# Optimization experiments

Measured on AMD Instinct MI355X. Metric: run time of the kernel, lower is better.

## Reference

```python
import jax, jax.numpy as jnp
import numpy as np

CODEBOOK_SIZE = 32768
EMBED_DIM = 4


def setup_inputs() -> dict:
    key = jax.random.key(0)
    k1, k2 = jax.random.split(key)
    # [batch, temporal, channels, height, width]
    hidden_state = jax.random.normal(k1, (1, 4, EMBED_DIM, 48, 48), dtype=jnp.float32)
    # nn.Embedding weight, init uniform(-1/cb, 1/cb) as in the torch module
    embedding = jax.random.uniform(
        k2, (CODEBOOK_SIZE, EMBED_DIM), dtype=jnp.float32,
        minval=-1.0 / CODEBOOK_SIZE, maxval=1.0 / CODEBOOK_SIZE,
    )
    return {"hidden_state": hidden_state, "embedding": embedding}


def reference(hidden_state, embedding):
    b, t, c, h, w = hidden_state.shape
    # permute channels last, flatten to [N, C]
    x = jnp.transpose(hidden_state, (0, 1, 3, 4, 2)).reshape(-1, c)
    distances = (
        jnp.sum(x * x, axis=1, keepdims=True)
        + jnp.sum(embedding * embedding, axis=1)
        - 2.0 * jnp.einsum("nd,kd->nk", x, embedding)
    )
    min_encoding_indices = jnp.argmin(distances, axis=1)
    return min_encoding_indices.reshape(b, t, h, w)
```

## Files before the change

### kernel.cpp

```cpp
#include <hip/hip_runtime.h>
#include <cfloat>


#define ROWS   9
#define BLOCK  256
#define NK     32768
#define EPT    2
#define CHUNK  (BLOCK * EPT)

__global__ __launch_bounds__(BLOCK, 2)
void vq_argmin_kernel(const float* __restrict__ hs,
                      const float4* __restrict__ cb,
                      int* __restrict__ out)
{
    __shared__ float sRD[4 * ROWS];
    __shared__ int   sRI[4 * ROWS];

    const int tid = threadIdx.x;
    const int rowbase = blockIdx.x * ROWS;

    float xr0[ROWS], xr1[ROWS], xr2[ROWS], xr3[ROWS];
    float x2[ROWS];
    float best[ROWS];
    int   bidx[ROWS];

    #pragma unroll
    for (int r = 0; r < ROWS; ++r) {
        int n = rowbase + r;
        int t = n / 2304;
        int rem = n - t * 2304;
        const float* p = hs + t * 9216 + rem;
        float a0 = p[0], a1 = p[2304], a2 = p[4608], a3 = p[6912];
        xr0[r] = a0; xr1[r] = a1; xr2[r] = a2; xr3[r] = a3;
        x2[r] = __fadd_rn(__fadd_rn(__fadd_rn(__fmul_rn(a0, a0),
                                              __fmul_rn(a1, a1)),
                                    __fmul_rn(a2, a2)),
                          __fmul_rn(a3, a3));
        best[r] = FLT_MAX;
        bidx[r] = 0;
    }

    float4 bufA[EPT], bufB[EPT];

    auto load_chunk = [&](float4* buf, int tb) {
        #pragma unroll
        for (int j = 0; j < EPT; ++j) buf[j] = cb[tb + tid + j * BLOCK];
    };
    auto compute_chunk = [&](const float4* buf, int tb) {
        #pragma unroll
        for (int j = 0; j < EPT; ++j) {
            float4 e = buf[j];
            float e2v = __fadd_rn(__fadd_rn(__fadd_rn(__fmul_rn(e.x, e.x),
                                                      __fmul_rn(e.y, e.y)),
                                            __fmul_rn(e.z, e.z)),
                                  __fmul_rn(e.w, e.w));
            int kk = tb + tid + j * BLOCK;
            #pragma unroll
            for (int r = 0; r < ROWS; ++r) {
                float dot = __builtin_fmaf(xr3[r], e.w,
                            __builtin_fmaf(xr2[r], e.z,
                            __builtin_fmaf(xr1[r], e.y,
                            __fmul_rn(xr0[r], e.x))));
                float t1 = __fadd_rn(x2[r], e2v);
                float d  = __builtin_fmaf(dot, -2.0f, t1);
                if (d < best[r]) { best[r] = d; bidx[r] = kk; }
            }
        }
    };

    load_chunk(bufA, 0);
    for (int tb = 0; tb < NK; tb += 2 * CHUNK) {
        load_chunk(bufB, tb + CHUNK);
        compute_chunk(bufA, tb);
        int nb = tb + 2 * CHUNK < NK ? tb + 2 * CHUNK : 0;
        load_chunk(bufA, nb);
        compute_chunk(bufB, tb + CHUNK);
    }

    #pragma unroll
    for (int r = 0; r < ROWS; ++r) {
        float d = best[r]; int i = bidx[r];
        #pragma unroll
        for (int off = 32; off >= 1; off >>= 1) {
            float d2 = __shfl_xor(d, off, 64);
            int   i2 = __shfl_xor(i, off, 64);
            if (d2 < d || (d2 == d && i2 < i)) { d = d2; i = i2; }
        }
        best[r] = d; bidx[r] = i;
    }

    int wave = tid >> 6;
    if ((tid & 63) == 0) {
        #pragma unroll
        for (int r = 0; r < ROWS; ++r) {
            sRD[wave * ROWS + r] = best[r];
            sRI[wave * ROWS + r] = bidx[r];
        }
    }
    __syncthreads();

    if (tid < ROWS) {
        float d = sRD[tid]; int i = sRI[tid];
        #pragma unroll
        for (int w = 1; w < 4; ++w) {
            float d2 = sRD[w * ROWS + tid];
            int   i2 = sRI[w * ROWS + tid];
            if (d2 < d || (d2 == d && i2 < i)) { d = d2; i = i2; }
        }
        out[rowbase + tid] = i;
    }
}

extern "C" void kernel_launch(void* const* d_in, const int* in_sizes, int n_in,
                              void* d_out, int out_size, void* d_ws, size_t ws_size,
                              hipStream_t stream)
{
    const float*  hs = (const float*)d_in[0];
    const float4* cb = (const float4*)d_in[1];
    int* out = (int*)d_out;

    const int nrows = 9216;
    dim3 grid(nrows / ROWS), block(BLOCK);
    vq_argmin_kernel<<<grid, block, 0, stream>>>(hs, cb, out);
}
```

Measured before the change: 125.0 us.

## Use packed FP32 math for row pairs and raise rows per block

Packs two query rows into 2-wide float vectors so the dot product and distance math can use packed FP32 FMA instructions. Query values are made wave-uniform via readfirstlane so they can live in scalar registers. The chunk slot is stored in place of the full codebook index, which is rebuilt after the loop. Rows per block rise from 9 to 12 and the occupancy hint changes to 3-4 waves per EU. The aim is fewer VALU instructions per distance, traded against more register pressure and a smaller grid.

```diff
diff --git a/kernel.cpp b/kernel.cpp
--- a/kernel.cpp
+++ b/kernel.cpp
@@ -2,13 +2,22 @@
 #include <cfloat>
 
 
-#define ROWS   9
-#define BLOCK  256
-#define NK     32768
-#define EPT    2
-#define CHUNK  (BLOCK * EPT)
+typedef float v2f __attribute__((ext_vector_type(2)));
 
-__global__ __launch_bounds__(BLOCK, 2)
+#define ROWS  12
+#define RP    (ROWS / 2)
+#define BLOCK 256
+#define NK    32768
+#define EPT   2
+#define CHUNK (BLOCK * EPT)
+
+__device__ __forceinline__ float rlf(float v) {
+    return __builtin_bit_cast(float,
+        __builtin_amdgcn_readfirstlane(__builtin_bit_cast(int, v)));
+}
+
+__global__ __launch_bounds__(BLOCK)
+__attribute__((amdgpu_waves_per_eu(3, 4)))
 void vq_argmin_kernel(const float* __restrict__ hs,
                       const float4* __restrict__ cb,
                       int* __restrict__ out)
@@ -19,26 +28,34 @@
     const int tid = threadIdx.x;
     const int rowbase = blockIdx.x * ROWS;
 
-    float xr0[ROWS], xr1[ROWS], xr2[ROWS], xr3[ROWS];
-    float x2[ROWS];
+    v2f xp0[RP], xp1[RP], xp2[RP], xp3[RP], x2p[RP];
     float best[ROWS];
     int   bidx[ROWS];
 
     #pragma unroll
-    for (int r = 0; r < ROWS; ++r) {
-        int n = rowbase + r;
-        int t = n / 2304;
-        int rem = n - t * 2304;
-        const float* p = hs + t * 9216 + rem;
-        float a0 = p[0], a1 = p[2304], a2 = p[4608], a3 = p[6912];
-        xr0[r] = a0; xr1[r] = a1; xr2[r] = a2; xr3[r] = a3;
-        x2[r] = __fadd_rn(__fadd_rn(__fadd_rn(__fmul_rn(a0, a0),
-                                              __fmul_rn(a1, a1)),
-                                    __fmul_rn(a2, a2)),
-                          __fmul_rn(a3, a3));
-        best[r] = FLT_MAX;
-        bidx[r] = 0;
+    for (int p = 0; p < RP; ++p) {
+        float c0[2], c1[2], c2[2], c3[2], q[2];
+        #pragma unroll
+        for (int h = 0; h < 2; ++h) {
+            int n = rowbase + 2 * p + h;
+            int t = n / 2304;
+            int rem = n - t * 2304;
+            const float* ptr = hs + t * 9216 + rem;
+            float a0 = ptr[0], a1 = ptr[2304], a2 = ptr[4608], a3 = ptr[6912];
+            c0[h] = a0; c1[h] = a1; c2[h] = a2; c3[h] = a3;
+            q[h] = __fadd_rn(__fadd_rn(__fadd_rn(__fmul_rn(a0, a0),
+                                                 __fmul_rn(a1, a1)),
+                                       __fmul_rn(a2, a2)),
+                             __fmul_rn(a3, a3));
+        }
+        xp0[p] = (v2f){rlf(c0[0]), rlf(c0[1])};
+        xp1[p] = (v2f){rlf(c1[0]), rlf(c1[1])};
+        xp2[p] = (v2f){rlf(c2[0]), rlf(c2[1])};
+        xp3[p] = (v2f){rlf(c3[0]), rlf(c3[1])};
+        x2p[p] = (v2f){rlf(q[0]),  rlf(q[1])};
     }
+    #pragma unroll
+    for (int r = 0; r < ROWS; ++r) { best[r] = FLT_MAX; bidx[r] = 0; }
 
     float4 bufA[EPT], bufB[EPT];
 
@@ -50,20 +67,24 @@
         #pragma unroll
         for (int j = 0; j < EPT; ++j) {
             float4 e = buf[j];
-            float e2v = __fadd_rn(__fadd_rn(__fadd_rn(__fmul_rn(e.x, e.x),
-                                                      __fmul_rn(e.y, e.y)),
-                                            __fmul_rn(e.z, e.z)),
-                                  __fmul_rn(e.w, e.w));
-            int kk = tb + tid + j * BLOCK;
+            float e2 = __fadd_rn(__fadd_rn(__fadd_rn(__fmul_rn(e.x, e.x),
+                                                     __fmul_rn(e.y, e.y)),
+                                           __fmul_rn(e.z, e.z)),
+                                 __fmul_rn(e.w, e.w));
+            v2f ex = {e.x, e.x}, ey = {e.y, e.y};
+            v2f ez = {e.z, e.z}, ew = {e.w, e.w};
+            v2f e2s = {e2, e2};
+            int m = tb / BLOCK + j;
             #pragma unroll
-            for (int r = 0; r < ROWS; ++r) {
-                float dot = __builtin_fmaf(xr3[r], e.w,
-                            __builtin_fmaf(xr2[r], e.z,
-                            __builtin_fmaf(xr1[r], e.y,
-                            __fmul_rn(xr0[r], e.x))));
-                float t1 = __fadd_rn(x2[r], e2v);
-                float d  = __builtin_fmaf(dot, -2.0f, t1);
-                if (d < best[r]) { best[r] = d; bidx[r] = kk; }
+            for (int p = 0; p < RP; ++p) {
+                v2f dot = xp0[p] * ex;
+                dot = __builtin_elementwise_fma(xp1[p], ey, dot);
+                dot = __builtin_elementwise_fma(xp2[p], ez, dot);
+                dot = __builtin_elementwise_fma(xp3[p], ew, dot);
+                v2f t1 = x2p[p] + e2s;
+                v2f d  = __builtin_elementwise_fma(dot, (v2f){-2.f, -2.f}, t1);
+                if (d.x < best[2 * p])     { best[2 * p] = d.x;     bidx[2 * p] = m; }
+                if (d.y < best[2 * p + 1]) { best[2 * p + 1] = d.y; bidx[2 * p + 1] = m; }
             }
         }
     };
@@ -77,16 +98,20 @@
         compute_chunk(bufB, tb + CHUNK);
     }
 
+    int kk[ROWS];
+    #pragma unroll
+    for (int r = 0; r < ROWS; ++r) kk[r] = bidx[r] * BLOCK + tid;
+
     #pragma unroll
     for (int r = 0; r < ROWS; ++r) {
-        float d = best[r]; int i = bidx[r];
+        float d = best[r]; int i = kk[r];
         #pragma unroll
         for (int off = 32; off >= 1; off >>= 1) {
             float d2 = __shfl_xor(d, off, 64);
             int   i2 = __shfl_xor(i, off, 64);
             if (d2 < d || (d2 == d && i2 < i)) { d = d2; i = i2; }
         }
-        best[r] = d; bidx[r] = i;
+        best[r] = d; kk[r] = i;
     }
 
     int wave = tid >> 6;
@@ -94,7 +119,7 @@
         #pragma unroll
         for (int r = 0; r < ROWS; ++r) {
             sRD[wave * ROWS + r] = best[r];
-            sRI[wave * ROWS + r] = bidx[r];
+            sRI[wave * ROWS + r] = kk[r];
         }
     }
     __syncthreads();
```

After: 121.1 us. 1.03x faster.
